# Performance work log

Hardware: AMD Instinct MI355X
Metric: run time of the kernel (lower is better)

Reference implementation:

```python
import jax, jax.numpy as jnp
import numpy as np
from jax import lax

K = 16  # number of KNN neighbors (fixed in module)


def _knn_neighbors(x, k):
    # x: (B, 3, N) point coordinates -> neighbor coords (B, 3, N, K)
    inner = jnp.einsum('bdn,bdm->bnm', x, x)          # (B, N, N)
    sq = jnp.sum(x * x, axis=1)                        # (B, N)
    d2 = sq[:, :, None] + sq[:, None, :] - 2.0 * inner  # pairwise sq dists (B, N, N)
    _, nbr_idx = lax.top_k(-d2, k)                     # k nearest (incl. self), (B, N, K)
    # gather neighbor coordinates: expand x to (B, 3, 1, N), idx to (B, 1, N, K)
    neighbor = jnp.take_along_axis(x[:, :, None, :], nbr_idx[:, None, :, :], axis=3)
    return neighbor  # (B, 3, N, K)


def _down_index(neighbor, x, npts_ds):
    # center-diff saliency: sum of squared offsets to K neighbors per point
    diff = neighbor - x[:, :, :, None]                 # (B, 3, N, K)
    score = jnp.sum(diff * diff, axis=(1, 3))          # (B, N)
    _, idx = lax.top_k(score, npts_ds)                 # (B, npts_ds)
    return idx


def setup_inputs() -> dict:
    key = jax.random.key(0)
    k1, k2 = jax.random.split(key)
    B, N, C = 8, 4096, 128
    x = jax.random.normal(k1, (B, 3, N), dtype=jnp.float32)
    y = jax.random.normal(k2, (B, C, N), dtype=jnp.float32)
    return {"x": x, "y": y, "npts_ds": 2048}


def reference(x, y, npts_ds):
    B, _, N = x.shape
    C = y.shape[1]
    neighbor = _knn_neighbors(x, K)                    # ops.group(x, K, 'neighbor')
    idx = _down_index(neighbor, x, npts_ds)            # ops.down_index(...), (B, npts_ds)
    idx3 = jnp.broadcast_to(idx[:, None, :], (B, 3, npts_ds))
    idxC = jnp.broadcast_to(idx[:, None, :], (B, C, npts_ds))
    top_k_xyz = jnp.take_along_axis(x, idx3, axis=2)    # (B, 3, npts_ds)
    top_k_points = jnp.take_along_axis(y, idxC, axis=2)  # (B, C, npts_ds)
    return (top_k_xyz, top_k_points)
```

## Files before the change

kernel.cpp:

```cpp
#include <hip/hip_runtime.h>
#include <math.h>

#define BATCH 8
#define NPTS 4096
#define CHAN 128
#define KNN 16
#define SPLIT 4
#define CHUNK (NPTS / SPLIT)
#define ISPLIT 4
#define QCH (CHUNK / ISPLIT)
#define PTILE 128
#define EPC 24
#define RSPLIT 4
#define RCHUNK (NPTS / RSPLIT)

typedef unsigned long long u64;

__device__ __forceinline__ u64 pack_key(float d2, int idx) {
  unsigned b = __float_as_uint(d2);
  b ^= (unsigned)((int)b >> 31) | 0x80000000u;
  return ((u64)b << 32) | (unsigned)idx;
}

__device__ __forceinline__ float d2_ref(float4 q, float ppx, float ppy,
                                        float ppz, float psq) {
  float inner = __fadd_rn(__fadd_rn(__fmul_rn(ppx, q.x), __fmul_rn(ppy, q.y)),
                          __fmul_rn(ppz, q.z));
  return __fsub_rn(__fadd_rn(psq, q.w), __fmul_rn(2.0f, inner));
}

__device__ __forceinline__ void ce_asc(u64& x, u64& y) {
  bool sw = y < x;
  u64 lo = sw ? y : x;
  u64 hi = sw ? x : y;
  x = lo;
  y = hi;
}

__device__ __forceinline__ void batcher_sort16_u64(u64 a[16]) {
#define CE(i, j) ce_asc(a[i], a[j])
  CE(0, 8); CE(1, 9); CE(2, 10); CE(3, 11);
  CE(4, 12); CE(5, 13); CE(6, 14); CE(7, 15);
  CE(0, 4); CE(1, 5); CE(2, 6); CE(3, 7);
  CE(8, 12); CE(9, 13); CE(10, 14); CE(11, 15);
  CE(4, 8); CE(5, 9); CE(6, 10); CE(7, 11);
  CE(0, 2); CE(1, 3); CE(4, 6); CE(5, 7);
  CE(8, 10); CE(9, 11); CE(12, 14); CE(13, 15);
  CE(2, 8); CE(3, 9); CE(6, 12); CE(7, 13);
  CE(2, 4); CE(3, 5); CE(6, 8); CE(7, 9); CE(10, 12); CE(11, 13);
  CE(0, 1); CE(2, 3); CE(4, 5); CE(6, 7);
  CE(8, 9); CE(10, 11); CE(12, 13); CE(14, 15);
  CE(1, 8); CE(3, 10); CE(5, 12); CE(7, 14);
  CE(1, 4); CE(3, 6); CE(5, 8); CE(7, 10); CE(9, 12); CE(11, 14);
  CE(1, 2); CE(3, 4); CE(5, 6); CE(7, 8); CE(9, 10); CE(11, 12); CE(13, 14);
#undef CE
}

__device__ __forceinline__ void bitonic_sort32(u64 a[32]) {
#pragma unroll
  for (int k = 2; k <= 32; k <<= 1) {
#pragma unroll
    for (int j = k >> 1; j > 0; j >>= 1) {
#pragma unroll
      for (int i = 0; i < 32; ++i) {
        int l = i ^ j;
        if (l > i) {
          if ((i & k) == 0) ce_asc(a[i], a[l]);
          else              ce_asc(a[l], a[i]);
        }
      }
    }
  }
}

__device__ __forceinline__ void merge_keep16(u64 T[16], const u64 A[16]) {
  u64 nt[16];
#pragma unroll
  for (int i = 0; i < 16; ++i) {
    u64 a = A[15 - i];
    nt[i] = (a < T[i]) ? a : T[i];
  }
#pragma unroll
  for (int j = 8; j > 0; j >>= 1) {
#pragma unroll
    for (int i = 0; i < 16; ++i) {
      int l = i ^ j;
      if (l > i) ce_asc(nt[i], nt[l]);
    }
  }
#pragma unroll
  for (int i = 0; i < 16; ++i) T[i] = nt[i];
}

__device__ __forceinline__ void ce_i32(int& x, int& y) {
  int lo = (x < y) ? x : y;
  int hi = (x < y) ? y : x;
  x = lo;
  y = hi;
}

__device__ __forceinline__ void batcher_sort16_i32(int a[16]) {
#define CE(i, j) ce_i32(a[i], a[j])
  CE(0, 8); CE(1, 9); CE(2, 10); CE(3, 11);
  CE(4, 12); CE(5, 13); CE(6, 14); CE(7, 15);
  CE(0, 4); CE(1, 5); CE(2, 6); CE(3, 7);
  CE(8, 12); CE(9, 13); CE(10, 14); CE(11, 15);
  CE(4, 8); CE(5, 9); CE(6, 10); CE(7, 11);
  CE(0, 2); CE(1, 3); CE(4, 6); CE(5, 7);
  CE(8, 10); CE(9, 11); CE(12, 14); CE(13, 15);
  CE(2, 8); CE(3, 9); CE(6, 12); CE(7, 13);
  CE(2, 4); CE(3, 5); CE(6, 8); CE(7, 9); CE(10, 12); CE(11, 13);
  CE(0, 1); CE(2, 3); CE(4, 5); CE(6, 7);
  CE(8, 9); CE(10, 11); CE(12, 13); CE(14, 15);
  CE(1, 8); CE(3, 10); CE(5, 12); CE(7, 14);
  CE(1, 4); CE(3, 6); CE(5, 8); CE(7, 10); CE(9, 12); CE(11, 14);
  CE(1, 2); CE(3, 4); CE(5, 6); CE(7, 8); CE(9, 10); CE(11, 12); CE(13, 14);
#undef CE
}

__device__ __forceinline__ void merge_keep16_i32(int T[16], const int A[16]) {
  int nt[16];
#pragma unroll
  for (int i = 0; i < 16; ++i) {
    int a = A[15 - i];
    nt[i] = (a < T[i]) ? a : T[i];
  }
#pragma unroll
  for (int j = 8; j > 0; j >>= 1) {
#pragma unroll
    for (int i = 0; i < 16; ++i) {
      int l = i ^ j;
      if (l > i) ce_i32(nt[i], nt[l]);
    }
  }
#pragma unroll
  for (int i = 0; i < 16; ++i) T[i] = nt[i];
}

__global__ __launch_bounds__(512) void knn_partial_kernel(
    const float* __restrict__ x, u64* __restrict__ pkey) {
  const int s = blockIdx.x % SPLIT;
  const int ntile = (blockIdx.x / SPLIT) % (NPTS / PTILE);
  const int b = blockIdx.x / (SPLIT * (NPTS / PTILE));
  const int p = threadIdx.x & (PTILE - 1);
  const int q4 = threadIdx.x >> 7;
  __shared__ float4 xs[CHUNK];
  __shared__ u64 ubuf[2048];

  const float* xb = x + (size_t)b * 3 * NPTS;
  for (int i = threadIdx.x; i < CHUNK; i += 512) {
    int gm = s * CHUNK + i;
    float px = xb[gm];
    float py = xb[NPTS + gm];
    float pz = xb[2 * NPTS + gm];
    float sq = __fadd_rn(__fadd_rn(__fmul_rn(px, px), __fmul_rn(py, py)),
                         __fmul_rn(pz, pz));
    xs[i] = make_float4(px, py, pz, sq);
  }

  const int n = ntile * PTILE + p;
  float ppx = xb[n];
  float ppy = xb[NPTS + n];
  float ppz = xb[2 * NPTS + n];
  float psq = __fadd_rn(__fadd_rn(__fmul_rn(ppx, ppx), __fmul_rn(ppy, ppy)),
                        __fmul_rn(ppz, ppz));
  __syncthreads();

  const int cbase = q4 * QCH;

  int T[16];
#pragma unroll
  for (int i = 0; i < 16; ++i) T[i] = 0x7FFFFFFF;
  int r17 = 0x7FFFFFFF;

#pragma unroll 1
  for (int base = 0; base < QCH; base += 16) {
    int A[16];
#pragma unroll
    for (int t = 0; t < 16; ++t) {
      float4 q = xs[cbase + base + t];
      int bits = __float_as_int(d2_ref(q, ppx, ppy, ppz, psq));
      A[t] = (bits & 0xFFFFFF00) | (base + t);
    }
    batcher_sort16_i32(A);
    int u[16];
#pragma unroll
    for (int i = 0; i < 16; ++i) {
      int a = A[15 - i];
      u[i] = (T[i] < a) ? a : T[i];
    }
#pragma unroll
    for (int w = 8; w > 0; w >>= 1) {
#pragma unroll
      for (int i = 0; i < 16; ++i) {
        if (i < w) u[i] = (u[i] < u[i + w]) ? u[i] : u[i + w];
      }
    }
    r17 = (r17 < u[0]) ? r17 : u[0];
    merge_keep16_i32(T, A);
  }

  const int tau = T[15] & 0xFFFFFF00;
  const bool slow = ((r17 & 0xFFFFFF00) == tau);

  u64 K[16];
  if (!slow) {
#pragma unroll
    for (int j = 0; j < 16; ++j) {
      int loc = cbase + (T[j] & 255);
      float4 q = xs[loc];
      float d2 = d2_ref(q, ppx, ppy, ppz, psq);
      K[j] = pack_key(d2, s * CHUNK + loc);
    }
    batcher_sort16_u64(K);
  } else {
    unsigned char* myb =
        reinterpret_cast<unsigned char*>(ubuf) + (unsigned)threadIdx.x * EPC;
    int cnt = 0;
#pragma unroll 4
    for (int m = 0; m < QCH; ++m) {
      float4 q = xs[cbase + m];
      int tb = __float_as_int(d2_ref(q, ppx, ppy, ppz, psq)) & 0xFFFFFF00;
      if (tb <= tau) {
        myb[cnt < EPC - 1 ? cnt : EPC - 1] = (unsigned char)m;
        ++cnt;
      }
    }
    u64 KK[32];
#pragma unroll
    for (int j = 0; j < EPC; ++j) {
      int loc = cbase + myb[j];
      float4 q = xs[loc];
      float d2 = d2_ref(q, ppx, ppy, ppz, psq);
      u64 k = pack_key(d2, s * CHUNK + loc);
      KK[j] = (j < cnt) ? k : ~0ull;
    }
#pragma unroll
    for (int j = EPC; j < 32; ++j) KK[j] = ~0ull;
    bitonic_sort32(KK);
#pragma unroll
    for (int j = 0; j < 16; ++j) K[j] = KK[j];
  }

  __syncthreads();
  u64(*L)[PTILE] = reinterpret_cast<u64(*)[PTILE]>(ubuf);
#pragma unroll 1
  for (int r = 1; r <= 3; ++r) {
    if (q4 == r) {
#pragma unroll
      for (int j = 0; j < 16; ++j) L[j][p] = K[j];
    }
    __syncthreads();
    if (q4 == 0) {
      u64 A64[16];
#pragma unroll
      for (int j = 0; j < 16; ++j) A64[j] = L[j][p];
      merge_keep16(K, A64);
    }
    __syncthreads();
  }
  if (q4 == 0) {
    u64* pb = pkey + ((size_t)(b * SPLIT + s) * KNN) * NPTS + n;
#pragma unroll
    for (int j = 0; j < 16; ++j) pb[(size_t)j * NPTS] = K[j];
  }
}

__global__ __launch_bounds__(64) void merge_score_kernel(
    const float* __restrict__ x, const u64* __restrict__ pkey,
    float* __restrict__ score, int* __restrict__ cnt) {
  const int b = blockIdx.x / (NPTS / 64);
  const int n = (blockIdx.x % (NPTS / 64)) * 64 + threadIdx.x;

  cnt[(size_t)b * NPTS + n] = 0;

  u64 T[16];
  {
    const u64* pb = pkey + ((size_t)(b * SPLIT + 0) * KNN) * NPTS + n;
#pragma unroll
    for (int j = 0; j < 16; ++j) T[j] = pb[(size_t)j * NPTS];
  }
#pragma unroll
  for (int s = 1; s < SPLIT; ++s) {
    const u64* pb = pkey + ((size_t)(b * SPLIT + s) * KNN) * NPTS + n;
    u64 A[16];
#pragma unroll
    for (int j = 0; j < 16; ++j) A[j] = pb[(size_t)j * NPTS];
    merge_keep16(T, A);
  }

  const float* xb = x + (size_t)b * 3 * NPTS;
  float ppx = xb[n];
  float ppy = xb[NPTS + n];
  float ppz = xb[2 * NPTS + n];

  float nx[KNN], ny[KNN], nz[KNN];
#pragma unroll
  for (int j = 0; j < KNN; ++j) {
    int idx = (int)(unsigned)T[j];
    nx[j] = xb[idx];
    ny[j] = xb[NPTS + idx];
    nz[j] = xb[2 * NPTS + idx];
  }

  float P[3];
#pragma unroll
  for (int d = 0; d < 3; ++d) {
    const float pc = (d == 0) ? ppx : ((d == 1) ? ppy : ppz);
    float r[8];
#pragma unroll
    for (int j = 0; j < 8; ++j) {
      float c0 = (d == 0) ? nx[j] : ((d == 1) ? ny[j] : nz[j]);
      float c1 = (d == 0) ? nx[j + 8] : ((d == 1) ? ny[j + 8] : nz[j + 8]);
      float e0 = __fsub_rn(c0, pc);
      float e1 = __fsub_rn(c1, pc);
      r[j] = __fadd_rn(__fmul_rn(e0, e0), __fmul_rn(e1, e1));
    }
    float t0 = __fadd_rn(r[0], r[1]);
    float t1 = __fadd_rn(r[2], r[3]);
    float t2 = __fadd_rn(r[4], r[5]);
    float t3 = __fadd_rn(r[6], r[7]);
    P[d] = __fadd_rn(__fadd_rn(t0, t1), __fadd_rn(t2, t3));
  }
  score[(size_t)b * NPTS + n] =
      __fadd_rn(__fadd_rn(P[0], P[1]), P[2]);
}

__global__ __launch_bounds__(256) void rank_partial_kernel(
    const float* __restrict__ score, int* __restrict__ cnt) {
  const int s = blockIdx.x % RSPLIT;
  const int ntile = (blockIdx.x / RSPLIT) % (NPTS / 256);
  const int b = blockIdx.x / (RSPLIT * (NPTS / 256));
  __shared__ float ss[RCHUNK];

  const float* sb = score + (size_t)b * NPTS;
  for (int i = threadIdx.x; i < RCHUNK; i += 256)
    ss[i] = sb[s * RCHUNK + i];

  const int n = ntile * 256 + threadIdx.x;
  const float sn = sb[n];
  __syncthreads();

  int c = 0;
#pragma unroll 8
  for (int mm = 0; mm < RCHUNK; ++mm) {
    float sm = ss[mm];
    int gm = s * RCHUNK + mm;
    c += (sm > sn) || (sm == sn && gm < n);
  }
  atomicAdd(&cnt[(size_t)b * NPTS + n], c);
}

__global__ __launch_bounds__(256) void rank_scatter_kernel(
    const int* __restrict__ cnt, int* __restrict__ sel, int npts) {
  int t = blockIdx.x * 256 + threadIdx.x;
  int b = t / NPTS;
  int n = t % NPTS;
  int c = cnt[t];
  if (c < npts) sel[(size_t)b * npts + c] = n;
}

__global__ __launch_bounds__(256) void gather_kernel(
    const float* __restrict__ x, const float* __restrict__ y,
    const int* __restrict__ sel, float* __restrict__ out, int npts,
    int total0, int total) {
  int tid = blockIdx.x * blockDim.x + threadIdx.x;
  if (tid >= total) return;
  if (tid < total0) {
    int j = tid % npts;
    int rest = tid / npts;
    int d = rest % 3;
    int b = rest / 3;
    int src = sel[b * npts + j];
    out[tid] = x[((size_t)b * 3 + d) * NPTS + src];
  } else {
    int t = tid - total0;
    int j = t % npts;
    int rest = t / npts;
    int c = rest % CHAN;
    int b = rest / CHAN;
    int src = sel[b * npts + j];
    out[tid] = y[((size_t)b * CHAN + c) * NPTS + src];
  }
}

extern "C" void kernel_launch(void* const* d_in, const int* in_sizes, int n_in,
                              void* d_out, int out_size, void* d_ws,
                              size_t ws_size, hipStream_t stream) {
  const float* x = (const float*)d_in[0];
  const float* y = (const float*)d_in[1];
  float* out = (float*)d_out;

  const int npts = out_size / (BATCH * (3 + CHAN));

  char* w = (char*)d_ws;
  u64* pkey = (u64*)w;
  w += sizeof(u64) * (size_t)BATCH * SPLIT * KNN * NPTS;
  float* score = (float*)w;
  w += sizeof(float) * (size_t)BATCH * NPTS;
  int* cnt = (int*)w;
  w += sizeof(int) * (size_t)BATCH * NPTS;
  int* sel = (int*)w;

  knn_partial_kernel<<<BATCH * (NPTS / PTILE) * SPLIT, 512, 0, stream>>>(
      x, pkey);
  merge_score_kernel<<<BATCH * NPTS / 64, 64, 0, stream>>>(x, pkey, score,
                                                           cnt);
  rank_partial_kernel<<<BATCH * (NPTS / 256) * RSPLIT, 256, 0, stream>>>(
      score, cnt);
  rank_scatter_kernel<<<BATCH * NPTS / 256, 256, 0, stream>>>(cnt, sel, npts);

  const int total0 = BATCH * 3 * npts;
  gather_kernel<<<(out_size + 255) / 256, 256, 0, stream>>>(
      x, y, sel, out, npts, total0, out_size);
}
```

Measured before the change: 250.1 us.

## Parallelize split merge across lanes with shuffles and vectorize rank loop

The merge/score kernel now gives each point four lanes, each loading one split's 16 candidate keys. A butterfly of two xor-shuffle merges combines them, and each of three lanes computes one coordinate's squared offsets, which are then summed with shuffles. This cuts the serial merge chain and per-thread register pressure, at the price of redundant merges on every lane. The rank kernel also reads scores from shared memory as float4 to reduce LDS instruction count.

```diff
diff --git a/kernel.cpp b/kernel.cpp
--- a/kernel.cpp
+++ b/kernel.cpp
@@ -266,52 +266,45 @@
   }
 }
 
-__global__ __launch_bounds__(64) void merge_score_kernel(
+__global__ __launch_bounds__(256) void merge_score_kernel(
     const float* __restrict__ x, const u64* __restrict__ pkey,
     float* __restrict__ score, int* __restrict__ cnt) {
+  const int tile = blockIdx.x % (NPTS / 64);
   const int b = blockIdx.x / (NPTS / 64);
-  const int n = (blockIdx.x % (NPTS / 64)) * 64 + threadIdx.x;
-
-  cnt[(size_t)b * NPTS + n] = 0;
+  const int g = threadIdx.x >> 2;
+  const int s = threadIdx.x & 3;
+  const int n = tile * 64 + g;
+
+  if (threadIdx.x < 64)
+    cnt[(size_t)b * NPTS + tile * 64 + threadIdx.x] = 0;
 
   u64 T[16];
   {
-    const u64* pb = pkey + ((size_t)(b * SPLIT + 0) * KNN) * NPTS + n;
+    const u64* pb = pkey + ((size_t)(b * SPLIT + s) * KNN) * NPTS + n;
 #pragma unroll
     for (int j = 0; j < 16; ++j) T[j] = pb[(size_t)j * NPTS];
   }
-#pragma unroll
-  for (int s = 1; s < SPLIT; ++s) {
-    const u64* pb = pkey + ((size_t)(b * SPLIT + s) * KNN) * NPTS + n;
-    u64 A[16];
-#pragma unroll
-    for (int j = 0; j < 16; ++j) A[j] = pb[(size_t)j * NPTS];
-    merge_keep16(T, A);
-  }
+
+  u64 A[16];
+#pragma unroll
+  for (int j = 0; j < 16; ++j)
+    A[j] = (u64)__shfl_xor((long long)T[j], 1);
+  merge_keep16(T, A);
+#pragma unroll
+  for (int j = 0; j < 16; ++j)
+    A[j] = (u64)__shfl_xor((long long)T[j], 2);
+  merge_keep16(T, A);
 
   const float* xb = x + (size_t)b * 3 * NPTS;
-  float ppx = xb[n];
-  float ppy = xb[NPTS + n];
-  float ppz = xb[2 * NPTS + n];
-
-  float nx[KNN], ny[KNN], nz[KNN];
-#pragma unroll
-  for (int j = 0; j < KNN; ++j) {
-    int idx = (int)(unsigned)T[j];
-    nx[j] = xb[idx];
-    ny[j] = xb[NPTS + idx];
-    nz[j] = xb[2 * NPTS + idx];
-  }
-
-  float P[3];
-#pragma unroll
-  for (int d = 0; d < 3; ++d) {
-    const float pc = (d == 0) ? ppx : ((d == 1) ? ppy : ppz);
+  float P = 0.0f;
+  if (s < 3) {
+    const float* xd = xb + (size_t)s * NPTS;
+    const float pc = xd[n];
     float r[8];
 #pragma unroll
     for (int j = 0; j < 8; ++j) {
-      float c0 = (d == 0) ? nx[j] : ((d == 1) ? ny[j] : nz[j]);
-      float c1 = (d == 0) ? nx[j + 8] : ((d == 1) ? ny[j + 8] : nz[j + 8]);
+      float c0 = xd[(int)(unsigned)T[j]];
+      float c1 = xd[(int)(unsigned)T[j + 8]];
       float e0 = __fsub_rn(c0, pc);
       float e1 = __fsub_rn(c1, pc);
       r[j] = __fadd_rn(__fmul_rn(e0, e0), __fmul_rn(e1, e1));
@@ -320,10 +313,12 @@
     float t1 = __fadd_rn(r[2], r[3]);
     float t2 = __fadd_rn(r[4], r[5]);
     float t3 = __fadd_rn(r[6], r[7]);
-    P[d] = __fadd_rn(__fadd_rn(t0, t1), __fadd_rn(t2, t3));
-  }
-  score[(size_t)b * NPTS + n] =
-      __fadd_rn(__fadd_rn(P[0], P[1]), P[2]);
+    P = __fadd_rn(__fadd_rn(t0, t1), __fadd_rn(t2, t3));
+  }
+  float Pa = __shfl_xor(P, 1);
+  float Pb = __shfl_xor(P, 2);
+  if (s == 0)
+    score[(size_t)b * NPTS + n] = __fadd_rn(__fadd_rn(P, Pa), Pb);
 }
 
 __global__ __launch_bounds__(256) void rank_partial_kernel(
@@ -331,22 +326,25 @@
   const int s = blockIdx.x % RSPLIT;
   const int ntile = (blockIdx.x / RSPLIT) % (NPTS / 256);
   const int b = blockIdx.x / (RSPLIT * (NPTS / 256));
-  __shared__ float ss[RCHUNK];
+  __shared__ float4 sv[RCHUNK / 4];
 
   const float* sb = score + (size_t)b * NPTS;
-  for (int i = threadIdx.x; i < RCHUNK; i += 256)
-    ss[i] = sb[s * RCHUNK + i];
+  const float4* sb4 = reinterpret_cast<const float4*>(sb + s * RCHUNK);
+  for (int i = threadIdx.x; i < RCHUNK / 4; i += 256) sv[i] = sb4[i];
 
   const int n = ntile * 256 + threadIdx.x;
   const float sn = sb[n];
   __syncthreads();
 
   int c = 0;
-#pragma unroll 8
-  for (int mm = 0; mm < RCHUNK; ++mm) {
-    float sm = ss[mm];
-    int gm = s * RCHUNK + mm;
-    c += (sm > sn) || (sm == sn && gm < n);
+#pragma unroll 4
+  for (int v = 0; v < RCHUNK / 4; ++v) {
+    float4 f = sv[v];
+    int gm = s * RCHUNK + 4 * v;
+    c += (f.x > sn) || (f.x == sn && gm < n);
+    c += (f.y > sn) || (f.y == sn && gm + 1 < n);
+    c += (f.z > sn) || (f.z == sn && gm + 2 < n);
+    c += (f.w > sn) || (f.w == sn && gm + 3 < n);
   }
   atomicAdd(&cnt[(size_t)b * NPTS + n], c);
 }
@@ -404,8 +402,8 @@
 
   knn_partial_kernel<<<BATCH * (NPTS / PTILE) * SPLIT, 512, 0, stream>>>(
       x, pkey);
-  merge_score_kernel<<<BATCH * NPTS / 64, 64, 0, stream>>>(x, pkey, score,
-                                                           cnt);
+  merge_score_kernel<<<BATCH * (NPTS / 64), 256, 0, stream>>>(x, pkey, score,
+                                                              cnt);
   rank_partial_kernel<<<BATCH * (NPTS / 256) * RSPLIT, 256, 0, stream>>>(
       score, cnt);
   rank_scatter_kernel<<<BATCH * NPTS / 256, 256, 0, stream>>>(cnt, sel, npts);
```

After: 246.9 us. No clear change (-1.3%).

## Fuse KNN split-merge and scoring into one kernel, fuse rank partials

Applied to the files above, without the earlier changes.

The KNN kernel now loads all 4096 points of a batch into shared memory and splits the candidate range across 16 thread groups of 32 points each. It merges their partial top-16 lists with an in-block tree reduction and computes the saliency score directly, removing the global partial-key buffer and the separate merge kernel. The rank step drops the atomic-based split and does the full count per block with two halves combined in shared memory, so the separate scatter kernel goes away too. Each KNN block now stages 64KB of shared memory and re-stages every point once per 32-query tile, which limits occupancy and adds redundant loads.

```diff
diff --git a/kernel.cpp b/kernel.cpp
--- a/kernel.cpp
+++ b/kernel.cpp
@@ -5,14 +5,10 @@
 #define NPTS 4096
 #define CHAN 128
 #define KNN 16
-#define SPLIT 4
-#define CHUNK (NPTS / SPLIT)
-#define ISPLIT 4
-#define QCH (CHUNK / ISPLIT)
-#define PTILE 128
+#define PTILE 32
+#define NGRP 16
+#define QCH (NPTS / NGRP)
 #define EPC 24
-#define RSPLIT 4
-#define RCHUNK (NPTS / RSPLIT)
 
 typedef unsigned long long u64;
 
@@ -137,36 +133,31 @@
   for (int i = 0; i < 16; ++i) T[i] = nt[i];
 }
 
-__global__ __launch_bounds__(512) void knn_partial_kernel(
-    const float* __restrict__ x, u64* __restrict__ pkey) {
-  const int s = blockIdx.x % SPLIT;
-  const int ntile = (blockIdx.x / SPLIT) % (NPTS / PTILE);
-  const int b = blockIdx.x / (SPLIT * (NPTS / PTILE));
+__global__ __launch_bounds__(512) void knn_score_kernel(
+    const float* __restrict__ x, float* __restrict__ score) {
+  const int ntile = blockIdx.x % (NPTS / PTILE);
+  const int b = blockIdx.x / (NPTS / PTILE);
   const int p = threadIdx.x & (PTILE - 1);
-  const int q4 = threadIdx.x >> 7;
-  __shared__ float4 xs[CHUNK];
-  __shared__ u64 ubuf[2048];
+  const int g = threadIdx.x >> 5;
+  __shared__ float4 xs[NPTS];
+  __shared__ unsigned char scratch[512 * EPC];
 
   const float* xb = x + (size_t)b * 3 * NPTS;
-  for (int i = threadIdx.x; i < CHUNK; i += 512) {
-    int gm = s * CHUNK + i;
-    float px = xb[gm];
-    float py = xb[NPTS + gm];
-    float pz = xb[2 * NPTS + gm];
+  for (int i = threadIdx.x; i < NPTS; i += 512) {
+    float px = xb[i];
+    float py = xb[NPTS + i];
+    float pz = xb[2 * NPTS + i];
     float sq = __fadd_rn(__fadd_rn(__fmul_rn(px, px), __fmul_rn(py, py)),
                          __fmul_rn(pz, pz));
     xs[i] = make_float4(px, py, pz, sq);
   }
+  __syncthreads();
 
   const int n = ntile * PTILE + p;
-  float ppx = xb[n];
-  float ppy = xb[NPTS + n];
-  float ppz = xb[2 * NPTS + n];
-  float psq = __fadd_rn(__fadd_rn(__fmul_rn(ppx, ppx), __fmul_rn(ppy, ppy)),
-                        __fmul_rn(ppz, ppz));
-  __syncthreads();
-
-  const int cbase = q4 * QCH;
+  float4 pp = xs[n];
+  const float ppx = pp.x, ppy = pp.y, ppz = pp.z, psq = pp.w;
+
+  const int cbase = g * QCH;
 
   int T[16];
 #pragma unroll
@@ -210,12 +201,11 @@
       int loc = cbase + (T[j] & 255);
       float4 q = xs[loc];
       float d2 = d2_ref(q, ppx, ppy, ppz, psq);
-      K[j] = pack_key(d2, s * CHUNK + loc);
+      K[j] = pack_key(d2, loc);
     }
     batcher_sort16_u64(K);
   } else {
-    unsigned char* myb =
-        reinterpret_cast<unsigned char*>(ubuf) + (unsigned)threadIdx.x * EPC;
+    unsigned char* myb = scratch + (unsigned)threadIdx.x * EPC;
     int cnt = 0;
 #pragma unroll 4
     for (int m = 0; m < QCH; ++m) {
@@ -232,7 +222,7 @@
       int loc = cbase + myb[j];
       float4 q = xs[loc];
       float d2 = d2_ref(q, ppx, ppy, ppz, psq);
-      u64 k = pack_key(d2, s * CHUNK + loc);
+      u64 k = pack_key(d2, loc);
       KK[j] = (j < cnt) ? k : ~0ull;
     }
 #pragma unroll
@@ -243,121 +233,93 @@
   }
 
   __syncthreads();
-  u64(*L)[PTILE] = reinterpret_cast<u64(*)[PTILE]>(ubuf);
+  u64* stg = reinterpret_cast<u64*>(xs);
+#pragma unroll
+  for (int j = 0; j < 16; ++j) stg[(g * 16 + j) * PTILE + p] = K[j];
+  __syncthreads();
 #pragma unroll 1
-  for (int r = 1; r <= 3; ++r) {
-    if (q4 == r) {
-#pragma unroll
-      for (int j = 0; j < 16; ++j) L[j][p] = K[j];
+  for (int r = 8; r >= 1; r >>= 1) {
+    if (g < r) {
+      u64 A64[16];
+#pragma unroll
+      for (int j = 0; j < 16; ++j)
+        A64[j] = stg[((g + r) * 16 + j) * PTILE + p];
+      merge_keep16(K, A64);
+      if (r > 1) {
+#pragma unroll
+        for (int j = 0; j < 16; ++j) stg[(g * 16 + j) * PTILE + p] = K[j];
+      }
     }
     __syncthreads();
-    if (q4 == 0) {
-      u64 A64[16];
-#pragma unroll
-      for (int j = 0; j < 16; ++j) A64[j] = L[j][p];
-      merge_keep16(K, A64);
-    }
-    __syncthreads();
-  }
-  if (q4 == 0) {
-    u64* pb = pkey + ((size_t)(b * SPLIT + s) * KNN) * NPTS + n;
-#pragma unroll
-    for (int j = 0; j < 16; ++j) pb[(size_t)j * NPTS] = K[j];
-  }
-}
-
-__global__ __launch_bounds__(64) void merge_score_kernel(
-    const float* __restrict__ x, const u64* __restrict__ pkey,
-    float* __restrict__ score, int* __restrict__ cnt) {
-  const int b = blockIdx.x / (NPTS / 64);
-  const int n = (blockIdx.x % (NPTS / 64)) * 64 + threadIdx.x;
-
-  cnt[(size_t)b * NPTS + n] = 0;
-
-  u64 T[16];
-  {
-    const u64* pb = pkey + ((size_t)(b * SPLIT + 0) * KNN) * NPTS + n;
-#pragma unroll
-    for (int j = 0; j < 16; ++j) T[j] = pb[(size_t)j * NPTS];
-  }
-#pragma unroll
-  for (int s = 1; s < SPLIT; ++s) {
-    const u64* pb = pkey + ((size_t)(b * SPLIT + s) * KNN) * NPTS + n;
-    u64 A[16];
-#pragma unroll
-    for (int j = 0; j < 16; ++j) A[j] = pb[(size_t)j * NPTS];
-    merge_keep16(T, A);
-  }
-
-  const float* xb = x + (size_t)b * 3 * NPTS;
-  float ppx = xb[n];
-  float ppy = xb[NPTS + n];
-  float ppz = xb[2 * NPTS + n];
-
-  float nx[KNN], ny[KNN], nz[KNN];
-#pragma unroll
-  for (int j = 0; j < KNN; ++j) {
-    int idx = (int)(unsigned)T[j];
-    nx[j] = xb[idx];
-    ny[j] = xb[NPTS + idx];
-    nz[j] = xb[2 * NPTS + idx];
-  }
-
-  float P[3];
-#pragma unroll
-  for (int d = 0; d < 3; ++d) {
-    const float pc = (d == 0) ? ppx : ((d == 1) ? ppy : ppz);
-    float r[8];
-#pragma unroll
-    for (int j = 0; j < 8; ++j) {
-      float c0 = (d == 0) ? nx[j] : ((d == 1) ? ny[j] : nz[j]);
-      float c1 = (d == 0) ? nx[j + 8] : ((d == 1) ? ny[j + 8] : nz[j + 8]);
-      float e0 = __fsub_rn(c0, pc);
-      float e1 = __fsub_rn(c1, pc);
-      r[j] = __fadd_rn(__fmul_rn(e0, e0), __fmul_rn(e1, e1));
-    }
-    float t0 = __fadd_rn(r[0], r[1]);
-    float t1 = __fadd_rn(r[2], r[3]);
-    float t2 = __fadd_rn(r[4], r[5]);
-    float t3 = __fadd_rn(r[6], r[7]);
-    P[d] = __fadd_rn(__fadd_rn(t0, t1), __fadd_rn(t2, t3));
-  }
-  score[(size_t)b * NPTS + n] =
-      __fadd_rn(__fadd_rn(P[0], P[1]), P[2]);
-}
-
-__global__ __launch_bounds__(256) void rank_partial_kernel(
-    const float* __restrict__ score, int* __restrict__ cnt) {
-  const int s = blockIdx.x % RSPLIT;
-  const int ntile = (blockIdx.x / RSPLIT) % (NPTS / 256);
-  const int b = blockIdx.x / (RSPLIT * (NPTS / 256));
-  __shared__ float ss[RCHUNK];
+  }
+
+  if (g == 0) {
+    float nx[KNN], ny[KNN], nz[KNN];
+#pragma unroll
+    for (int j = 0; j < KNN; ++j) {
+      int idx = (int)(unsigned)K[j];
+      nx[j] = xb[idx];
+      ny[j] = xb[NPTS + idx];
+      nz[j] = xb[2 * NPTS + idx];
+    }
+    float P[3];
+#pragma unroll
+    for (int d = 0; d < 3; ++d) {
+      const float pc = (d == 0) ? ppx : ((d == 1) ? ppy : ppz);
+      float r[8];
+#pragma unroll
+      for (int j = 0; j < 8; ++j) {
+        float c0 = (d == 0) ? nx[j] : ((d == 1) ? ny[j] : nz[j]);
+        float c1 = (d == 0) ? nx[j + 8] : ((d == 1) ? ny[j + 8] : nz[j + 8]);
+        float e0 = __fsub_rn(c0, pc);
+        float e1 = __fsub_rn(c1, pc);
+        r[j] = __fadd_rn(__fmul_rn(e0, e0), __fmul_rn(e1, e1));
+      }
+      float t0 = __fadd_rn(r[0], r[1]);
+      float t1 = __fadd_rn(r[2], r[3]);
+      float t2 = __fadd_rn(r[4], r[5]);
+      float t3 = __fadd_rn(r[6], r[7]);
+      P[d] = __fadd_rn(__fadd_rn(t0, t1), __fadd_rn(t2, t3));
+    }
+    score[(size_t)b * NPTS + n] =
+        __fadd_rn(__fadd_rn(P[0], P[1]), P[2]);
+  }
+}
+
+__global__ __launch_bounds__(256) void rank_scatter_kernel(
+    const float* __restrict__ score, int* __restrict__ sel, int npts) {
+  const int tile = blockIdx.x % (NPTS / 128);
+  const int b = blockIdx.x / (NPTS / 128);
+  const int p = threadIdx.x & 127;
+  const int h = threadIdx.x >> 7;
+  __shared__ float4 sv[NPTS / 4];
+  __shared__ int cpart[128];
 
   const float* sb = score + (size_t)b * NPTS;
-  for (int i = threadIdx.x; i < RCHUNK; i += 256)
-    ss[i] = sb[s * RCHUNK + i];
-
-  const int n = ntile * 256 + threadIdx.x;
+  const float4* sb4 = reinterpret_cast<const float4*>(sb);
+  for (int i = threadIdx.x; i < NPTS / 4; i += 256) sv[i] = sb4[i];
+
+  const int n = tile * 128 + p;
   const float sn = sb[n];
   __syncthreads();
 
   int c = 0;
-#pragma unroll 8
-  for (int mm = 0; mm < RCHUNK; ++mm) {
-    float sm = ss[mm];
-    int gm = s * RCHUNK + mm;
-    c += (sm > sn) || (sm == sn && gm < n);
-  }
-  atomicAdd(&cnt[(size_t)b * NPTS + n], c);
-}
-
-__global__ __launch_bounds__(256) void rank_scatter_kernel(
-    const int* __restrict__ cnt, int* __restrict__ sel, int npts) {
-  int t = blockIdx.x * 256 + threadIdx.x;
-  int b = t / NPTS;
-  int n = t % NPTS;
-  int c = cnt[t];
-  if (c < npts) sel[(size_t)b * npts + c] = n;
+  const int v0 = h * (NPTS / 8);
+#pragma unroll 4
+  for (int v = v0; v < v0 + NPTS / 8; ++v) {
+    float4 f = sv[v];
+    int gm = 4 * v;
+    c += (f.x > sn) || (f.x == sn && gm < n);
+    c += (f.y > sn) || (f.y == sn && gm + 1 < n);
+    c += (f.z > sn) || (f.z == sn && gm + 2 < n);
+    c += (f.w > sn) || (f.w == sn && gm + 3 < n);
+  }
+  if (h == 1) cpart[p] = c;
+  __syncthreads();
+  if (h == 0) {
+    c += cpart[p];
+    if (c < npts) sel[(size_t)b * npts + c] = n;
+  }
 }
 
 __global__ __launch_bounds__(256) void gather_kernel(
@@ -394,22 +356,13 @@
   const int npts = out_size / (BATCH * (3 + CHAN));
 
   char* w = (char*)d_ws;
-  u64* pkey = (u64*)w;
-  w += sizeof(u64) * (size_t)BATCH * SPLIT * KNN * NPTS;
   float* score = (float*)w;
   w += sizeof(float) * (size_t)BATCH * NPTS;
-  int* cnt = (int*)w;
-  w += sizeof(int) * (size_t)BATCH * NPTS;
   int* sel = (int*)w;
 
-  knn_partial_kernel<<<BATCH * (NPTS / PTILE) * SPLIT, 512, 0, stream>>>(
-      x, pkey);
-  merge_score_kernel<<<BATCH * NPTS / 64, 64, 0, stream>>>(x, pkey, score,
-                                                           cnt);
-  rank_partial_kernel<<<BATCH * (NPTS / 256) * RSPLIT, 256, 0, stream>>>(
-      score, cnt);
-  rank_scatter_kernel<<<BATCH * NPTS / 256, 256, 0, stream>>>(cnt, sel, npts);
-
+  knn_score_kernel<<<BATCH * (NPTS / PTILE), 512, 0, stream>>>(x, score);
+  rank_scatter_kernel<<<BATCH * (NPTS / 128), 256, 0, stream>>>(score, sel,
+                                                                npts);
   const int total0 = BATCH * 3 * npts;
   gather_kernel<<<(out_size + 255) / 256, 256, 0, stream>>>(
       x, y, sel, out, npts, total0, out_size);
```

Result: slower. 257.0 us (+2.7%).
